# Kernel optimization log

Measured on AMD Instinct MI355X. Metric: run time of the kernel, lower is better.

Reference implementation:

```python
import jax, jax.numpy as jnp
import numpy as np

DIM = 768
NUM_HEADS = 12
SCALE = 1.0 / (DIM ** 0.5)  # NOTE: source scales by 1/sqrt(dim), not 1/sqrt(head_dim)


def setup_inputs() -> dict:
    key = jax.random.key(0)
    k_x, k_qkv, k_ow, k_ob = jax.random.split(key, 4)
    b, n = 8, 1024
    x = jax.random.normal(k_x, (b, n, DIM), dtype=jnp.float32)
    # torch Linear weight is [out, in]; we store jax-style [in, out]
    w_qkv = jax.random.normal(k_qkv, (DIM, 3 * DIM), dtype=jnp.float32) * (DIM ** -0.5)
    w_out = jax.random.normal(k_ow, (DIM, DIM), dtype=jnp.float32) * (DIM ** -0.5)
    b_out = jax.random.normal(k_ob, (DIM,), dtype=jnp.float32) * 0.01
    return {"x": x, "w_qkv": w_qkv, "w_out": w_out, "b_out": b_out}


def reference(x, w_qkv, w_out, b_out):
    b, n, c = x.shape
    h = NUM_HEADS
    hd = c // h
    qkv = (x @ w_qkv).reshape(b, n, 3, h, hd)
    q, k, v = jnp.moveaxis(qkv, 2, 0)          # each [b, n, h, hd]
    q = jnp.swapaxes(q, 1, 2)                  # [b, h, n, hd]
    k = jnp.swapaxes(k, 1, 2)
    v = jnp.swapaxes(v, 1, 2)
    dot = jnp.einsum('bhqd,bhkd->bhqk', q, k) * SCALE
    attn = jax.nn.softmax(dot, axis=-1)        # attn_dropout p=0 -> identity
    out = jnp.einsum('bhqk,bhkd->bhqd', attn, v)
    out = jnp.swapaxes(out, 1, 2).reshape(b, n, c)
    return out @ w_out + b_out                 # proj_dropout p=0 -> identity
```

## Files before the change

### kernel.cpp

```cpp
#include <hip/hip_runtime.h>

#define DEV __device__ __forceinline__

typedef __bf16 bf16x8 __attribute__((ext_vector_type(8)));
typedef float  f32x4  __attribute__((ext_vector_type(4)));
typedef float  f32x16 __attribute__((ext_vector_type(16)));
typedef unsigned int u32x4 __attribute__((ext_vector_type(4)));

static constexpr float SCALE = 0.036084391824351615f;
static constexpr float L2E   = 1.4426950408889634f;

DEV unsigned short f2bf(float f) {
  return __builtin_bit_cast(unsigned short, (__bf16)f);
}
DEV unsigned int pack2(float a, float b) {
  return (unsigned int)f2bf(a) | ((unsigned int)f2bf(b) << 16);
}

#define GLDS16(gp, lp) \
  __builtin_amdgcn_global_load_lds((__attribute__((address_space(1))) void*)(gp), \
                                   (__attribute__((address_space(3))) void*)(lp), 16, 0, 0)


__global__ __launch_bounds__(256) void k_cvt_bf16(const float* __restrict__ in,
                                                  unsigned short* __restrict__ out,
                                                  int n8) {
  int i = blockIdx.x * 256 + threadIdx.x;
  if (i >= n8) return;
  const float4* p = (const float4*)in + (size_t)i * 2;
  float4 a = p[0], b = p[1];
  uint4 r;
  r.x = pack2(a.x, a.y); r.y = pack2(a.z, a.w);
  r.z = pack2(b.x, b.y); r.w = pack2(b.z, b.w);
  ((uint4*)out)[i] = r;
}

__global__ __launch_bounds__(256) void k_transpose_w(const float* __restrict__ in,
                                                     unsigned short* __restrict__ out,
                                                     int R, int C) {
  __shared__ float tile[64][65];
  int c0 = blockIdx.x * 64, r0 = blockIdx.y * 64;
  int t = threadIdx.x, tr = t >> 6, tc = t & 63;
#pragma unroll
  for (int i = 0; i < 64; i += 4)
    tile[i + tr][tc] = in[(size_t)(r0 + i + tr) * C + c0 + tc];
  __syncthreads();
#pragma unroll
  for (int i = 0; i < 64; i += 4)
    out[(size_t)(c0 + i + tr) * R + r0 + tc] = f2bf(tile[tc][i + tr]);
}

template <int MODE>
__global__ __launch_bounds__(256) void k_gemm(const unsigned short* __restrict__ A,
                                              const unsigned short* __restrict__ BT,
                                              void* __restrict__ out0,
                                              unsigned short* __restrict__ Kb,
                                              unsigned short* __restrict__ VTb,
                                              const float* __restrict__ bias) {
  __shared__ __align__(16) char smem[32768];
  char* As = smem;
  char* Bs = smem + 16384;
  const int tid = threadIdx.x;
  const int wave = tid >> 6, lane = tid & 63;
  const int g = lane >> 4, l15 = lane & 15;
  const int wrow = wave >> 1, wcol = wave & 1;

  int id = blockIdx.y * gridDim.x + blockIdx.x;
  int per_xcd = (gridDim.x * gridDim.y) >> 3;
  int id2 = (id & 7) * per_xcd + (id >> 3);
  const int bm = id2 / gridDim.x, bn = id2 % gridDim.x;

  f32x4 acc[4][4] = {};
  const unsigned short* Abase = A + (size_t)bm * 128 * 768;
  const unsigned short* Bbase = BT + (size_t)bn * 128 * 768;

  for (int kt = 0; kt < 12; ++kt) {
    const int k0 = kt * 64;
#pragma unroll
    for (int i = 0; i < 4; ++i) {
      int q = i * 256 + tid;
      int row = q >> 3, c = q & 7;
      int cs = c ^ (row & 7);
      GLDS16(Abase + (size_t)row * 768 + k0 + cs * 8, As + (i * 256 + wave * 64) * 16);
      GLDS16(Bbase + (size_t)row * 768 + k0 + cs * 8, Bs + (i * 256 + wave * 64) * 16);
    }
    __syncthreads();
    __builtin_amdgcn_s_setprio(1);
#pragma unroll
    for (int kk = 0; kk < 2; ++kk) {
      bf16x8 af[4], bfr[4];
#pragma unroll
      for (int mi = 0; mi < 4; ++mi) {
        int r = wrow * 64 + mi * 16 + l15;
        af[mi] = *(const bf16x8*)(As + r * 128 + (((kk * 4 + g) ^ (r & 7)) * 16));
      }
#pragma unroll
      for (int ni = 0; ni < 4; ++ni) {
        int r = wcol * 64 + ni * 16 + l15;
        bfr[ni] = *(const bf16x8*)(Bs + r * 128 + (((kk * 4 + g) ^ (r & 7)) * 16));
      }
#pragma unroll
      for (int mi = 0; mi < 4; ++mi)
#pragma unroll
        for (int ni = 0; ni < 4; ++ni)
          acc[mi][ni] = __builtin_amdgcn_mfma_f32_16x16x32_bf16(af[mi], bfr[ni], acc[mi][ni], 0, 0, 0);
    }
    __builtin_amdgcn_s_setprio(0);
    __syncthreads();
  }

  const int row0 = bm * 128 + wrow * 64;
  const int col0 = bn * 128 + wcol * 64;
#pragma unroll
  for (int mi = 0; mi < 4; ++mi) {
#pragma unroll
    for (int ni = 0; ni < 4; ++ni) {
      int col = col0 + ni * 16 + l15;
      if (MODE == 0) {
        int which = col / 768;
        int hd = col - which * 768;
        int head = hd >> 6, d = hd & 63;
        int rowm0 = row0 + mi * 16 + g * 4;
        int bi = rowm0 >> 10, np = rowm0 & 1023;
        if (which == 0) {
#pragma unroll
          for (int j = 0; j < 4; ++j)
            ((unsigned short*)out0)[((size_t)(bi * 12 + head) * 1024 + np + j) * 64 + d] =
                f2bf(acc[mi][ni][j] * (SCALE * L2E));
        } else if (which == 1) {
#pragma unroll
          for (int j = 0; j < 4; ++j)
            Kb[((size_t)(bi * 12 + head) * 1024 + np + j) * 64 + d] = f2bf(acc[mi][ni][j]);
        } else {
          ushort4 w;
          w.x = f2bf(acc[mi][ni][0]); w.y = f2bf(acc[mi][ni][1]);
          w.z = f2bf(acc[mi][ni][2]); w.w = f2bf(acc[mi][ni][3]);
          *(ushort4*)(VTb + ((size_t)(bi * 12 + head) * 64 + d) * 1024 + np) = w;
        }
      } else {
        float bz = bias[col];
#pragma unroll
        for (int j = 0; j < 4; ++j) {
          int rowm = row0 + mi * 16 + g * 4 + j;
          ((float*)out0)[(size_t)rowm * 768 + col] = acc[mi][ni][j] + bz;
        }
      }
    }
  }
}

__global__ __launch_bounds__(256) void k_attn(const unsigned short* __restrict__ Qb,
                                              const unsigned short* __restrict__ Kb,
                                              const unsigned short* __restrict__ VTb,
                                              unsigned short* __restrict__ Ao) {
  __shared__ __align__(16) char smem[32768];
  const int tid = threadIdx.x, wave = tid >> 6, lane = tid & 63;
  const int hi = lane >> 5, q31 = lane & 31;
  const int bh = blockIdx.x % 96, qt = blockIdx.x / 96;
  const int qbase = qt * 128 + wave * 32;
  const unsigned short* Kp = Kb + (size_t)bh * 65536;
  const unsigned short* Vp = VTb + (size_t)bh * 65536;

  auto STAGE = [&](int buf, int kt) {
#pragma unroll
    for (int i = 0; i < 2; ++i) {
      int q = i * 256 + tid;
      int row = q >> 3, c = q & 7;
      int cs = c ^ (row & 7);
      GLDS16(Kp + (size_t)(kt * 64 + row) * 64 + cs * 8,
             smem + buf * 8192 + (i * 256 + wave * 64) * 16);
      GLDS16(Vp + (size_t)row * 1024 + kt * 64 + cs * 8,
             smem + 16384 + buf * 8192 + (i * 256 + wave * 64) * 16);
    }
  };

  bf16x8 aq[4];
#pragma unroll
  for (int dk = 0; dk < 4; ++dk)
    aq[dk] = *(const bf16x8*)(Qb + (size_t)bh * 65536 +
                              (size_t)(qbase + q31) * 64 + dk * 16 + hi * 8);

  f32x16 o0 = {}, o1 = {};
  float lsum = 0.f;

  STAGE(0, 0);
  __syncthreads();
  int cur = 0;

  for (int kt = 0; kt < 16; ++kt) {
    if (kt < 15) STAGE(cur ^ 1, kt + 1);
    char* Ks = smem + cur * 8192;
    char* Vs = smem + 16384 + cur * 8192;

#pragma unroll
    for (int sub = 0; sub < 2; ++sub) {
      f32x16 st = {};
      __builtin_amdgcn_s_setprio(1);
#pragma unroll
      for (int dk = 0; dk < 4; ++dk) {
        int r = sub * 32 + q31;
        bf16x8 ka = *(const bf16x8*)(Ks + r * 128 + (((dk * 2 + hi) ^ (r & 7)) * 16));
        st = __builtin_amdgcn_mfma_f32_32x32x16_bf16(ka, aq[dk], st, 0, 0, 0);
      }
      __builtin_amdgcn_s_setprio(0);

      float ex[16];
#pragma unroll
      for (int r2 = 0; r2 < 16; ++r2) ex[r2] = __builtin_amdgcn_exp2f(st[r2]);
      float s0 = (ex[0] + ex[1]) + (ex[2] + ex[3]);
      float s1 = (ex[4] + ex[5]) + (ex[6] + ex[7]);
      float s2 = (ex[8] + ex[9]) + (ex[10] + ex[11]);
      float s3 = (ex[12] + ex[13]) + (ex[14] + ex[15]);
      lsum += (s0 + s1) + (s2 + s3);

      unsigned w00 = pack2(ex[0], ex[1]),   w01 = pack2(ex[2], ex[3]);
      unsigned w10 = pack2(ex[4], ex[5]),   w11 = pack2(ex[6], ex[7]);
      unsigned w20 = pack2(ex[8], ex[9]),   w21 = pack2(ex[10], ex[11]);
      unsigned w30 = pack2(ex[12], ex[13]), w31 = pack2(ex[14], ex[15]);
      unsigned r00 = __shfl_xor((int)w00, 32), r01 = __shfl_xor((int)w01, 32);
      unsigned r10 = __shfl_xor((int)w10, 32), r11 = __shfl_xor((int)w11, 32);
      unsigned r20 = __shfl_xor((int)w20, 32), r21 = __shfl_xor((int)w21, 32);
      unsigned r30 = __shfl_xor((int)w30, 32), r31 = __shfl_xor((int)w31, 32);

      __builtin_amdgcn_s_setprio(1);
#pragma unroll
      for (int s = 0; s < 2; ++s) {
        u32x4 au;
        if (s == 0) {
          au[0] = hi ? r10 : w00; au[1] = hi ? r11 : w01;
          au[2] = hi ? w10 : r00; au[3] = hi ? w11 : r01;
        } else {
          au[0] = hi ? r30 : w20; au[1] = hi ? r31 : w21;
          au[2] = hi ? w30 : r20; au[3] = hi ? w31 : r21;
        }
        bf16x8 pa = __builtin_bit_cast(bf16x8, au);
        int ch = sub * 4 + s * 2 + hi;
        int vr0 = q31, vr1 = 32 + q31;
        bf16x8 vb0 = *(const bf16x8*)(Vs + vr0 * 128 + ((ch ^ (vr0 & 7)) * 16));
        bf16x8 vb1 = *(const bf16x8*)(Vs + vr1 * 128 + ((ch ^ (vr1 & 7)) * 16));
        o0 = __builtin_amdgcn_mfma_f32_32x32x16_bf16(pa, vb0, o0, 0, 0, 0);
        o1 = __builtin_amdgcn_mfma_f32_32x32x16_bf16(pa, vb1, o1, 0, 0, 0);
      }
      __builtin_amdgcn_s_setprio(0);
    }

    __syncthreads();
    cur ^= 1;
  }

  lsum += __shfl_xor(lsum, 32);
  float linv = 1.0f / lsum;
  const int b_idx = bh / 12, h = bh - b_idx * 12;
#pragma unroll
  for (int m = 0; m < 4; ++m) {
#pragma unroll
    for (int j = 0; j < 4; ++j) {
      int qr = j + 8 * m + 4 * hi;
      float lj = __shfl(linv, qr);
      int reg = m * 4 + j;
      size_t base = (size_t)(b_idx * 1024 + qbase + qr) * 768 + h * 64 + q31;
      Ao[base]      = f2bf(o0[reg] * lj);
      Ao[base + 32] = f2bf(o1[reg] * lj);
    }
  }
}


extern "C" void kernel_launch(void* const* d_in, const int* in_sizes, int n_in,
                              void* d_out, int out_size, void* d_ws, size_t ws_size,
                              hipStream_t stream) {
  const float* x     = (const float*)d_in[0];
  const float* w_qkv = (const float*)d_in[1];
  const float* w_out = (const float*)d_in[2];
  const float* b_out = (const float*)d_in[3];

  char* ws = (char*)d_ws;
  size_t off = 0;
  auto alloc = [&](size_t bytes) {
    void* p = ws + off;
    off += (bytes + 255) & ~(size_t)255;
    return p;
  };
  unsigned short* xb    = (unsigned short*)alloc(8192ull * 768 * 2);
  unsigned short* wqkvT = (unsigned short*)alloc(2304ull * 768 * 2);
  unsigned short* woutT = (unsigned short*)alloc(768ull * 768 * 2);
  unsigned short* Qb    = (unsigned short*)alloc(96ull * 1024 * 64 * 2);
  unsigned short* Kbf   = (unsigned short*)alloc(96ull * 1024 * 64 * 2);
  unsigned short* VTb   = (unsigned short*)alloc(96ull * 1024 * 64 * 2);
  unsigned short* Aob   = (unsigned short*)alloc(96ull * 1024 * 64 * 2);

  k_cvt_bf16<<<3072, 256, 0, stream>>>(x, xb, 786432);
  k_transpose_w<<<dim3(36, 12), 256, 0, stream>>>(w_qkv, wqkvT, 768, 2304);
  k_transpose_w<<<dim3(12, 12), 256, 0, stream>>>(w_out, woutT, 768, 768);
  k_gemm<0><<<dim3(18, 64), 256, 0, stream>>>(xb, wqkvT, Qb, Kbf, VTb, nullptr);
  k_attn<<<768, 256, 0, stream>>>(Qb, Kbf, VTb, Aob);
  k_gemm<1><<<dim3(6, 64), 256, 0, stream>>>(Aob, woutT, d_out, nullptr, nullptr, b_out);
}
```

Before: 112.5 us.

## Replace LDS-staged K/V tiles with direct register double-buffered global loads in attention

The attention kernel drops the shared-memory double buffer filled with global_load_lds and the per-tile __syncthreads. Each wave now loads its K and V^T fragments straight from global memory into registers, with a two-deep software pipeline over 32-key chunks. Launch bounds are raised to ask for 3 blocks per CU. This removes LDS traffic and block-wide barriers, but the four waves of a block now each fetch the same K/V data from L2/L1 separately, and global-load latency may be harder to hide.

```diff
diff --git a/kernel.cpp b/kernel.cpp
--- a/kernel.cpp
+++ b/kernel.cpp
@@ -149,11 +149,10 @@
   }
 }
 
-__global__ __launch_bounds__(256) void k_attn(const unsigned short* __restrict__ Qb,
-                                              const unsigned short* __restrict__ Kb,
-                                              const unsigned short* __restrict__ VTb,
-                                              unsigned short* __restrict__ Ao) {
-  __shared__ __align__(16) char smem[32768];
+__global__ __launch_bounds__(256, 3) void k_attn(const unsigned short* __restrict__ Qb,
+                                                 const unsigned short* __restrict__ Kb,
+                                                 const unsigned short* __restrict__ VTb,
+                                                 unsigned short* __restrict__ Ao) {
   const int tid = threadIdx.x, wave = tid >> 6, lane = tid & 63;
   const int hi = lane >> 5, q31 = lane & 31;
   const int bh = blockIdx.x % 96, qt = blockIdx.x / 96;
@@ -161,19 +160,6 @@
   const unsigned short* Kp = Kb + (size_t)bh * 65536;
   const unsigned short* Vp = VTb + (size_t)bh * 65536;
 
-  auto STAGE = [&](int buf, int kt) {
-#pragma unroll
-    for (int i = 0; i < 2; ++i) {
-      int q = i * 256 + tid;
-      int row = q >> 3, c = q & 7;
-      int cs = c ^ (row & 7);
-      GLDS16(Kp + (size_t)(kt * 64 + row) * 64 + cs * 8,
-             smem + buf * 8192 + (i * 256 + wave * 64) * 16);
-      GLDS16(Vp + (size_t)row * 1024 + kt * 64 + cs * 8,
-             smem + 16384 + buf * 8192 + (i * 256 + wave * 64) * 16);
-    }
-  };
-
   bf16x8 aq[4];
 #pragma unroll
   for (int dk = 0; dk < 4; ++dk)
@@ -183,70 +169,70 @@
   f32x16 o0 = {}, o1 = {};
   float lsum = 0.f;
 
-  STAGE(0, 0);
-  __syncthreads();
-  int cur = 0;
-
-  for (int kt = 0; kt < 16; ++kt) {
-    if (kt < 15) STAGE(cur ^ 1, kt + 1);
-    char* Ks = smem + cur * 8192;
-    char* Vs = smem + 16384 + cur * 8192;
-
-#pragma unroll
-    for (int sub = 0; sub < 2; ++sub) {
-      f32x16 st = {};
-      __builtin_amdgcn_s_setprio(1);
-#pragma unroll
-      for (int dk = 0; dk < 4; ++dk) {
-        int r = sub * 32 + q31;
-        bf16x8 ka = *(const bf16x8*)(Ks + r * 128 + (((dk * 2 + hi) ^ (r & 7)) * 16));
-        st = __builtin_amdgcn_mfma_f32_32x32x16_bf16(ka, aq[dk], st, 0, 0, 0);
-      }
-      __builtin_amdgcn_s_setprio(0);
-
-      float ex[16];
-#pragma unroll
-      for (int r2 = 0; r2 < 16; ++r2) ex[r2] = __builtin_amdgcn_exp2f(st[r2]);
-      float s0 = (ex[0] + ex[1]) + (ex[2] + ex[3]);
-      float s1 = (ex[4] + ex[5]) + (ex[6] + ex[7]);
-      float s2 = (ex[8] + ex[9]) + (ex[10] + ex[11]);
-      float s3 = (ex[12] + ex[13]) + (ex[14] + ex[15]);
-      lsum += (s0 + s1) + (s2 + s3);
-
-      unsigned w00 = pack2(ex[0], ex[1]),   w01 = pack2(ex[2], ex[3]);
-      unsigned w10 = pack2(ex[4], ex[5]),   w11 = pack2(ex[6], ex[7]);
-      unsigned w20 = pack2(ex[8], ex[9]),   w21 = pack2(ex[10], ex[11]);
-      unsigned w30 = pack2(ex[12], ex[13]), w31 = pack2(ex[14], ex[15]);
-      unsigned r00 = __shfl_xor((int)w00, 32), r01 = __shfl_xor((int)w01, 32);
-      unsigned r10 = __shfl_xor((int)w10, 32), r11 = __shfl_xor((int)w11, 32);
-      unsigned r20 = __shfl_xor((int)w20, 32), r21 = __shfl_xor((int)w21, 32);
-      unsigned r30 = __shfl_xor((int)w30, 32), r31 = __shfl_xor((int)w31, 32);
-
-      __builtin_amdgcn_s_setprio(1);
-#pragma unroll
-      for (int s = 0; s < 2; ++s) {
-        u32x4 au;
-        if (s == 0) {
-          au[0] = hi ? r10 : w00; au[1] = hi ? r11 : w01;
-          au[2] = hi ? w10 : r00; au[3] = hi ? w11 : r01;
-        } else {
-          au[0] = hi ? r30 : w20; au[1] = hi ? r31 : w21;
-          au[2] = hi ? w30 : r20; au[3] = hi ? w31 : r21;
-        }
-        bf16x8 pa = __builtin_bit_cast(bf16x8, au);
-        int ch = sub * 4 + s * 2 + hi;
-        int vr0 = q31, vr1 = 32 + q31;
-        bf16x8 vb0 = *(const bf16x8*)(Vs + vr0 * 128 + ((ch ^ (vr0 & 7)) * 16));
-        bf16x8 vb1 = *(const bf16x8*)(Vs + vr1 * 128 + ((ch ^ (vr1 & 7)) * 16));
-        o0 = __builtin_amdgcn_mfma_f32_32x32x16_bf16(pa, vb0, o0, 0, 0, 0);
-        o1 = __builtin_amdgcn_mfma_f32_32x32x16_bf16(pa, vb1, o1, 0, 0, 0);
-      }
-      __builtin_amdgcn_s_setprio(0);
-    }
-
-    __syncthreads();
-    cur ^= 1;
-  }
+  const unsigned short* krow = Kp + (size_t)q31 * 64 + hi * 8;
+  const unsigned short* vrow0 = Vp + (size_t)q31 * 1024 + hi * 8;
+  const unsigned short* vrow1 = Vp + (size_t)(32 + q31) * 1024 + hi * 8;
+
+#define LOADKV(K_, V_, kt_)                                            \
+  {                                                                    \
+    const unsigned short* kp = krow + (size_t)(kt_) * 32 * 64;         \
+    K_[0] = *(const bf16x8*)(kp);                                      \
+    K_[1] = *(const bf16x8*)(kp + 16);                                 \
+    K_[2] = *(const bf16x8*)(kp + 32);                                 \
+    K_[3] = *(const bf16x8*)(kp + 48);                                 \
+    V_[0] = *(const bf16x8*)(vrow0 + (kt_) * 32);                      \
+    V_[1] = *(const bf16x8*)(vrow1 + (kt_) * 32);                      \
+    V_[2] = *(const bf16x8*)(vrow0 + (kt_) * 32 + 16);                 \
+    V_[3] = *(const bf16x8*)(vrow1 + (kt_) * 32 + 16);                 \
+  }
+
+#define COMPUTE(K_, V_)                                                \
+  {                                                                    \
+    f32x16 st = {};                                                    \
+    __builtin_amdgcn_s_setprio(1);                                     \
+    st = __builtin_amdgcn_mfma_f32_32x32x16_bf16(K_[0], aq[0], st, 0, 0, 0); \
+    st = __builtin_amdgcn_mfma_f32_32x32x16_bf16(K_[1], aq[1], st, 0, 0, 0); \
+    st = __builtin_amdgcn_mfma_f32_32x32x16_bf16(K_[2], aq[2], st, 0, 0, 0); \
+    st = __builtin_amdgcn_mfma_f32_32x32x16_bf16(K_[3], aq[3], st, 0, 0, 0); \
+    __builtin_amdgcn_s_setprio(0);                                     \
+    float ex[16];                                                      \
+    _Pragma("unroll")                                                  \
+    for (int r2 = 0; r2 < 16; ++r2) ex[r2] = __builtin_amdgcn_exp2f(st[r2]); \
+    lsum += ((ex[0] + ex[1]) + (ex[2] + ex[3])) + ((ex[4] + ex[5]) + (ex[6] + ex[7])) \
+          + ((ex[8] + ex[9]) + (ex[10] + ex[11])) + ((ex[12] + ex[13]) + (ex[14] + ex[15])); \
+    unsigned w0 = pack2(ex[0], ex[1]),   w1 = pack2(ex[2], ex[3]);     \
+    unsigned w2 = pack2(ex[4], ex[5]),   w3 = pack2(ex[6], ex[7]);     \
+    unsigned w4 = pack2(ex[8], ex[9]),   w5 = pack2(ex[10], ex[11]);   \
+    unsigned w6 = pack2(ex[12], ex[13]), w7 = pack2(ex[14], ex[15]);   \
+    unsigned r0 = __shfl_xor((int)w0, 32), r1 = __shfl_xor((int)w1, 32); \
+    unsigned r2_ = __shfl_xor((int)w2, 32), r3 = __shfl_xor((int)w3, 32); \
+    unsigned r4 = __shfl_xor((int)w4, 32), r5 = __shfl_xor((int)w5, 32); \
+    unsigned r6 = __shfl_xor((int)w6, 32), r7 = __shfl_xor((int)w7, 32); \
+    u32x4 a0, a1;                                                      \
+    if (hi) { a0[0] = r2_; a0[1] = r3; a0[2] = w2; a0[3] = w3;         \
+              a1[0] = r6;  a1[1] = r7; a1[2] = w6; a1[3] = w7; }       \
+    else    { a0[0] = w0; a0[1] = w1; a0[2] = r0; a0[3] = r1;          \
+              a1[0] = w4; a1[1] = w5; a1[2] = r4; a1[3] = r5; }        \
+    bf16x8 pa0 = __builtin_bit_cast(bf16x8, a0);                       \
+    bf16x8 pa1 = __builtin_bit_cast(bf16x8, a1);                       \
+    __builtin_amdgcn_s_setprio(1);                                     \
+    o0 = __builtin_amdgcn_mfma_f32_32x32x16_bf16(pa0, V_[0], o0, 0, 0, 0); \
+    o1 = __builtin_amdgcn_mfma_f32_32x32x16_bf16(pa0, V_[1], o1, 0, 0, 0); \
+    o0 = __builtin_amdgcn_mfma_f32_32x32x16_bf16(pa1, V_[2], o0, 0, 0, 0); \
+    o1 = __builtin_amdgcn_mfma_f32_32x32x16_bf16(pa1, V_[3], o1, 0, 0, 0); \
+    __builtin_amdgcn_s_setprio(0);                                     \
+  }
+
+  bf16x8 kA[4], vA[4], kB[4], vB[4];
+  LOADKV(kA, vA, 0);
+  for (int kt = 0; kt < 32; kt += 2) {
+    LOADKV(kB, vB, kt + 1);
+    COMPUTE(kA, vA);
+    if (kt + 2 < 32) LOADKV(kA, vA, kt + 2);
+    COMPUTE(kB, vB);
+  }
+#undef LOADKV
+#undef COMPUTE
 
   lsum += __shfl_xor(lsum, 32);
   float linv = 1.0f / lsum;
```

Measured after the change: 159.4 us. 41.7% more time.

## Transpose LDS tile layout, use permlane32_swap, and compute row sums via MFMA

Applied to the files above, without the earlier changes.

Restages K and V tiles into LDS in a chunk-major layout (chunk*64+row), so reads no longer need an XOR swizzle and each wave's global loads hit one column chunk across 64 rows. Swaps the eight cross-half shuffles for four permlane32_swap instructions. Computes softmax denominators with an extra MFMA against a ones vector instead of scalar adds and a final shuffle. This adds a third MFMA per PV step, and the new global access pattern is strided per lane, which may make global loads less coalesced.

```diff
diff --git a/kernel.cpp b/kernel.cpp
--- a/kernel.cpp
+++ b/kernel.cpp
@@ -164,12 +164,10 @@
   auto STAGE = [&](int buf, int kt) {
 #pragma unroll
     for (int i = 0; i < 2; ++i) {
-      int q = i * 256 + tid;
-      int row = q >> 3, c = q & 7;
-      int cs = c ^ (row & 7);
-      GLDS16(Kp + (size_t)(kt * 64 + row) * 64 + cs * 8,
+      int c = i * 4 + wave;
+      GLDS16(Kp + (size_t)(kt * 64 + lane) * 64 + c * 8,
              smem + buf * 8192 + (i * 256 + wave * 64) * 16);
-      GLDS16(Vp + (size_t)row * 1024 + kt * 64 + cs * 8,
+      GLDS16(Vp + (size_t)lane * 1024 + kt * 64 + c * 8,
              smem + 16384 + buf * 8192 + (i * 256 + wave * 64) * 16);
     }
   };
@@ -180,8 +178,12 @@
     aq[dk] = *(const bf16x8*)(Qb + (size_t)bh * 65536 +
                               (size_t)(qbase + q31) * 64 + dk * 16 + hi * 8);
 
+  bf16x8 vones;
+#pragma unroll
+  for (int e = 0; e < 8; ++e) vones[e] = (__bf16)1.0f;
+
   f32x16 o0 = {}, o1 = {};
-  float lsum = 0.f;
+  f32x16 lacc = {};
 
   STAGE(0, 0);
   __syncthreads();
@@ -198,8 +200,7 @@
       __builtin_amdgcn_s_setprio(1);
 #pragma unroll
       for (int dk = 0; dk < 4; ++dk) {
-        int r = sub * 32 + q31;
-        bf16x8 ka = *(const bf16x8*)(Ks + r * 128 + (((dk * 2 + hi) ^ (r & 7)) * 16));
+        bf16x8 ka = *(const bf16x8*)(Ks + (((dk * 2 + hi) * 64 + sub * 32 + q31) * 16));
         st = __builtin_amdgcn_mfma_f32_32x32x16_bf16(ka, aq[dk], st, 0, 0, 0);
       }
       __builtin_amdgcn_s_setprio(0);
@@ -207,39 +208,30 @@
       float ex[16];
 #pragma unroll
       for (int r2 = 0; r2 < 16; ++r2) ex[r2] = __builtin_amdgcn_exp2f(st[r2]);
-      float s0 = (ex[0] + ex[1]) + (ex[2] + ex[3]);
-      float s1 = (ex[4] + ex[5]) + (ex[6] + ex[7]);
-      float s2 = (ex[8] + ex[9]) + (ex[10] + ex[11]);
-      float s3 = (ex[12] + ex[13]) + (ex[14] + ex[15]);
-      lsum += (s0 + s1) + (s2 + s3);
 
       unsigned w00 = pack2(ex[0], ex[1]),   w01 = pack2(ex[2], ex[3]);
       unsigned w10 = pack2(ex[4], ex[5]),   w11 = pack2(ex[6], ex[7]);
       unsigned w20 = pack2(ex[8], ex[9]),   w21 = pack2(ex[10], ex[11]);
       unsigned w30 = pack2(ex[12], ex[13]), w31 = pack2(ex[14], ex[15]);
-      unsigned r00 = __shfl_xor((int)w00, 32), r01 = __shfl_xor((int)w01, 32);
-      unsigned r10 = __shfl_xor((int)w10, 32), r11 = __shfl_xor((int)w11, 32);
-      unsigned r20 = __shfl_xor((int)w20, 32), r21 = __shfl_xor((int)w21, 32);
-      unsigned r30 = __shfl_xor((int)w30, 32), r31 = __shfl_xor((int)w31, 32);
+
+      auto pA = __builtin_amdgcn_permlane32_swap(w00, w10, false, false);
+      auto pB = __builtin_amdgcn_permlane32_swap(w01, w11, false, false);
+      auto pC = __builtin_amdgcn_permlane32_swap(w20, w30, false, false);
+      auto pD = __builtin_amdgcn_permlane32_swap(w21, w31, false, false);
 
       __builtin_amdgcn_s_setprio(1);
 #pragma unroll
       for (int s = 0; s < 2; ++s) {
         u32x4 au;
-        if (s == 0) {
-          au[0] = hi ? r10 : w00; au[1] = hi ? r11 : w01;
-          au[2] = hi ? w10 : r00; au[3] = hi ? w11 : r01;
-        } else {
-          au[0] = hi ? r30 : w20; au[1] = hi ? r31 : w21;
-          au[2] = hi ? w30 : r20; au[3] = hi ? w31 : r21;
-        }
+        if (s == 0) { au[0] = pA[0]; au[1] = pB[0]; au[2] = pA[1]; au[3] = pB[1]; }
+        else        { au[0] = pC[0]; au[1] = pD[0]; au[2] = pC[1]; au[3] = pD[1]; }
         bf16x8 pa = __builtin_bit_cast(bf16x8, au);
         int ch = sub * 4 + s * 2 + hi;
-        int vr0 = q31, vr1 = 32 + q31;
-        bf16x8 vb0 = *(const bf16x8*)(Vs + vr0 * 128 + ((ch ^ (vr0 & 7)) * 16));
-        bf16x8 vb1 = *(const bf16x8*)(Vs + vr1 * 128 + ((ch ^ (vr1 & 7)) * 16));
-        o0 = __builtin_amdgcn_mfma_f32_32x32x16_bf16(pa, vb0, o0, 0, 0, 0);
-        o1 = __builtin_amdgcn_mfma_f32_32x32x16_bf16(pa, vb1, o1, 0, 0, 0);
+        bf16x8 vb0 = *(const bf16x8*)(Vs + (ch * 64 + q31) * 16);
+        bf16x8 vb1 = *(const bf16x8*)(Vs + (ch * 64 + 32 + q31) * 16);
+        o0   = __builtin_amdgcn_mfma_f32_32x32x16_bf16(pa, vb0, o0, 0, 0, 0);
+        o1   = __builtin_amdgcn_mfma_f32_32x32x16_bf16(pa, vb1, o1, 0, 0, 0);
+        lacc = __builtin_amdgcn_mfma_f32_32x32x16_bf16(pa, vones, lacc, 0, 0, 0);
       }
       __builtin_amdgcn_s_setprio(0);
     }
@@ -248,19 +240,17 @@
     cur ^= 1;
   }
 
-  lsum += __shfl_xor(lsum, 32);
-  float linv = 1.0f / lsum;
   const int b_idx = bh / 12, h = bh - b_idx * 12;
 #pragma unroll
   for (int m = 0; m < 4; ++m) {
 #pragma unroll
     for (int j = 0; j < 4; ++j) {
+      int reg = m * 4 + j;
       int qr = j + 8 * m + 4 * hi;
-      float lj = __shfl(linv, qr);
-      int reg = m * 4 + j;
+      float linv = 1.0f / lacc[reg];
       size_t base = (size_t)(b_idx * 1024 + qbase + qr) * 768 + h * 64 + q31;
-      Ao[base]      = f2bf(o0[reg] * lj);
-      Ao[base + 32] = f2bf(o1[reg] * lj);
+      Ao[base]      = f2bf(o0[reg] * linv);
+      Ao[base + 32] = f2bf(o1[reg] * linv);
     }
   }
 }
```

Result: no change. 110.4 us (-1.9%).
